# Optimization experiments

Hardware: AMD Instinct MI355X
Metric: run time of the kernel (lower is better)

Reference implementation:

```python
import jax, jax.numpy as jnp
import numpy as np

B, DIN, H, NACT = 8192, 1025, 1024, 1026
NHEAD = 513  # npatches + STOP
K = 32       # kR = kS


def _make_seq(key, batch, n, k):
    k_idx, k_len = jax.random.split(key)
    # distinct indices per row: top-k of a random permutation
    perm = jnp.argsort(jax.random.uniform(k_idx, (batch, n)), axis=1)[:, :k]
    seq_len = jax.random.randint(k_len, (batch,), 1, k + 1).astype(jnp.int32)
    mask = jnp.arange(k)[None, :] < seq_len[:, None]
    seq_idx = jnp.where(mask, perm, -1).astype(jnp.int32)
    return seq_idx, seq_len


def setup_inputs() -> dict:
    key = jax.random.key(0)
    ks = jax.random.split(key, 8)
    state = jax.random.normal(ks[0], (B, DIN), dtype=jnp.float32)
    W0 = jax.random.normal(ks[1], (DIN, H), dtype=jnp.float32) * (2.0 / DIN) ** 0.5
    b0 = jnp.zeros((H,), jnp.float32)
    W1 = jax.random.normal(ks[2], (H, H), dtype=jnp.float32) * (2.0 / H) ** 0.5
    b1 = jnp.zeros((H,), jnp.float32)
    W2 = jax.random.normal(ks[3], (H, NACT), dtype=jnp.float32) * 0.01
    b2 = jnp.zeros((NACT,), jnp.float32)
    seq_idx_R, seq_len_R = _make_seq(ks[4], B, NHEAD, K)
    seq_idx_S, seq_len_S = _make_seq(ks[5], B, NHEAD, K)
    return {"state": state, "W0": W0, "b0": b0, "W1": W1, "b1": b1,
            "W2": W2, "b2": b2,
            "seq_idx_R": seq_idx_R, "seq_len_R": seq_len_R,
            "seq_idx_S": seq_idx_S, "seq_len_S": seq_len_S}


def _mlp(state, W0, b0, W1, b1, W2, b2):
    h = jax.nn.relu(state @ W0 + b0)
    h = jax.nn.relu(h @ W1 + b1)
    return h @ W2 + b2  # (B, NACT) logits


def _logprob_entropy_wo_replacement(logits, seq_idx, seq_len):
    # Faithful vectorized version of logprob_entropy_wo_replacement_batched.
    bsz, n = logits.shape
    col = jnp.arange(n)[None, :]
    neg_inf = jnp.float32(-jnp.inf)

    def step(carry, xs):
        remaining, logp, ent = carry          # (B,N) bool, (B,), (B,)
        t, idx_t = xs                          # scalar, (B,)
        active = t < seq_len                   # (B,)
        masked_logits = jnp.where(remaining, logits, neg_inf)
        lp = jax.nn.log_softmax(masked_logits, axis=-1)
        p = jnp.exp(lp)
        mp = jnp.where(remaining, p, 0.0)
        mlp_ = jnp.where(remaining, lp, 0.0)
        ent_step = -jnp.sum(mp * mlp_, axis=-1)
        ent = ent + jnp.where(active, ent_step, 0.0)
        valid = active & (idx_t >= 0)
        idx_safe = jnp.where(valid, idx_t, 0)
        g = jnp.take_along_axis(lp, idx_safe[:, None], axis=1)[:, 0]
        logp = logp + jnp.where(valid, g, 0.0)
        hit = (col == idx_safe[:, None]) & valid[:, None]
        remaining = remaining & ~hit
        return (remaining, logp, ent), None

    init = (jnp.ones((bsz, n), bool), jnp.zeros((bsz,), jnp.float32),
            jnp.zeros((bsz,), jnp.float32))
    ts = jnp.arange(seq_idx.shape[1], dtype=jnp.int32)
    (_, logp, ent), _ = jax.lax.scan(step, init, (ts, seq_idx.T))
    return logp, ent


def reference(state, W0, b0, W1, b1, W2, b2,
              seq_idx_R, seq_len_R, seq_idx_S, seq_len_S):
    x = _mlp(state, W0, b0, W1, b1, W2, b2)
    logpR, entR = _logprob_entropy_wo_replacement(x[:, :NHEAD], seq_idx_R, seq_len_R)
    logpS, entS = _logprob_entropy_wo_replacement(x[:, NHEAD:NHEAD + NHEAD], seq_idx_S, seq_len_S)
    # rows: [total logprob, total entropy] as in get_log_prob's (logpR+logpS, entR+entS)
    return jnp.stack([logpR + logpS, entR + entS], axis=0)  # (2, B)
```

## Files before the change

### kernel.cpp

```cpp
#include <hip/hip_runtime.h>
#include <cstdint>
#include <cstddef>

#define BATCH 8192
#define DIN   1025
#define HID   1024
#define NACT  1026
#define NHEAD 513
#define KSEL  32
#define KP0   1088
#define LGN   1024

typedef unsigned short u16;
typedef short bf16x8 __attribute__((ext_vector_type(8)));
typedef float f32x4 __attribute__((ext_vector_type(4)));

__device__ __forceinline__ u16 f2bf(float f) {
  unsigned u = __float_as_uint(f);
  u += 0x7fff + ((u >> 16) & 1);
  return (u16)(u >> 16);
}
__device__ __forceinline__ float bf2f(u16 h) {
  return __uint_as_float((unsigned)h << 16);
}

__device__ __forceinline__ void async_cp16(const u16* g, u16* l) {
  __builtin_amdgcn_global_load_lds((const __attribute__((address_space(1))) void*)g,
                                   (__attribute__((address_space(3))) void*)l,
                                   16, 0, 0);
}

__global__ __launch_bounds__(512) void k_cvt(const float* __restrict__ state,
    const float* __restrict__ W0, const float* __restrict__ W1,
    const float* __restrict__ W2,
    u16* __restrict__ As, u16* __restrict__ W0t, u16* __restrict__ W1t,
    u16* __restrict__ W2t, u16* __restrict__ W2c) {
  const int tid = threadIdx.x;
  const int b = blockIdx.x;
  {
    int i = b * 512 + tid;
    const int QPR = KP0 / 4;
    int r = i / QPR, c4 = (i - r * QPR) * 4;
    const float* src = state + (size_t)r * DIN + c4;
    ushort4 o;
    if (c4 + 3 < DIN) {
      o.x = f2bf(src[0]); o.y = f2bf(src[1]); o.z = f2bf(src[2]); o.w = f2bf(src[3]);
    } else {
      o.x = (c4 + 0 < DIN) ? f2bf(src[0]) : 0;
      o.y = (c4 + 1 < DIN) ? f2bf(src[1]) : 0;
      o.z = (c4 + 2 < DIN) ? f2bf(src[2]) : 0;
      o.w = (c4 + 3 < DIN) ? f2bf(src[3]) : 0;
    }
    *(ushort4*)(As + (size_t)r * KP0 + c4) = o;
  }
  if (b >= 3137) return;
  if (b == 3136) {
    for (int e = tid; e < 2048; e += 512) {
      int j = e >> 10, k = e & 1023;
      W2c[e] = f2bf(W2[(size_t)k * NACT + 1024 + j]);
    }
    return;
  }
  const float* W; u16* Wt; int K, ldW, Kp, tt = b;
  if (tt < 1088)      { W = W0; Wt = W0t; K = DIN; ldW = HID;  Kp = KP0; }
  else if (tt < 2112) { tt -= 1088; W = W1; Wt = W1t; K = HID; ldW = HID;  Kp = HID; }
  else                { tt -= 2112; W = W2; Wt = W2t; K = HID; ldW = NACT; Kp = HID; }
  int n0 = (tt & 31) * 32, k0 = (tt >> 5) * 32;
  __shared__ float tile[32][33];
  const int tx = tid & 31, ty = tid >> 5;
#pragma unroll
  for (int i = 0; i < 32; i += 16) {
    int k = k0 + ty + i;
    tile[ty + i][tx] = (k < K) ? W[(size_t)k * ldW + n0 + tx] : 0.f;
  }
  __syncthreads();
#pragma unroll
  for (int i = 0; i < 32; i += 16)
    Wt[(size_t)(n0 + ty + i) * Kp + k0 + tx] = f2bf(tile[tx][ty + i]);
}

template<bool RELU, int K>
__global__ __launch_bounds__(256, 4)
void gemm_bt(const u16* __restrict__ A, const u16* __restrict__ Bt,
             const float* __restrict__ bias, u16* __restrict__ Cout, int ldc)
{
  __shared__ __align__(16) u16 lds[12288];

  const int d     = blockIdx.x;
  const int xcd   = d & 7;
  const int j     = d >> 3;
  const int mtile = (xcd << 3) | (j & 7);
  const int ntile = j >> 3;
  const size_t bm = (size_t)mtile * 128;
  const size_t bn = (size_t)ntile * 64;

  const int tid  = threadIdx.x;
  const int wave = tid >> 6;
  const int lane = tid & 63;
  const int waveM = wave >> 1, waveN = wave & 1;
  const int lr = lane & 15, lq = lane >> 4;

  const int row0 = tid >> 2;
  const int g_   = (tid & 3) ^ ((tid >> 3) & 3);
  const u16* gA0 = A  + (bm + row0) * (size_t)K + g_ * 8;
  const u16* gA1 = A  + (bm + row0 + 64) * (size_t)K + g_ * 8;
  const u16* gB0 = Bt + (bn + row0) * (size_t)K + g_ * 8;
  u16* lA0 = lds + wave * 512;
  u16* lA1 = lds + 2048 + wave * 512;
  u16* lB0 = lds + 4096 + wave * 512;

  f32x4 acc[4][2] = {};

  const int s = lq ^ ((lr >> 1) & 3);
  const u16* pa = lds + (waveM * 64 + lr) * 32 + s * 8;
  const u16* pb = lds + 4096 + (waveN * 32 + lr) * 32 + s * 8;

  auto issue = [&](int k0, int buf) {
    const int o = buf * 6144;
    async_cp16(gA0 + k0, lA0 + o);
    async_cp16(gA1 + k0, lA1 + o);
    async_cp16(gB0 + k0, lB0 + o);
  };

  const int NIT = K / 32;
  issue(0, 0);
#pragma unroll 2
  for (int it = 0; it < NIT; ++it) {
    const int buf = it & 1;
    if (it + 1 < NIT) {
      issue((it + 1) * 32, buf ^ 1);
      asm volatile("s_waitcnt vmcnt(3)\n\ts_barrier" ::: "memory");
    } else {
      asm volatile("s_waitcnt vmcnt(0)\n\ts_barrier" ::: "memory");
    }

    bf16x8 af[4], bfr[2];
    const u16* qa = pa + buf * 6144;
    const u16* qb = pb + buf * 6144;
#pragma unroll
    for (int t = 0; t < 4; ++t)
      af[t]  = *(const bf16x8*)(qa + t * 512);
#pragma unroll
    for (int t = 0; t < 2; ++t)
      bfr[t] = *(const bf16x8*)(qb + t * 512);
#pragma unroll
    for (int tm = 0; tm < 4; ++tm)
#pragma unroll
      for (int tn = 0; tn < 2; ++tn)
        acc[tm][tn] = __builtin_amdgcn_mfma_f32_16x16x32_bf16(af[tm], bfr[tn], acc[tm][tn], 0, 0, 0);

    asm volatile("s_waitcnt lgkmcnt(0)\n\ts_barrier" ::: "memory");
  }

#pragma unroll
  for (int tm = 0; tm < 4; ++tm) {
    size_t rw = bm + waveM * 64 + tm * 16 + lq * 4;
#pragma unroll
    for (int tn = 0; tn < 2; ++tn) {
      int col = (int)bn + waveN * 32 + tn * 16 + lr;
      float bv = bias[col];
#pragma unroll
      for (int r = 0; r < 4; ++r) {
        float v = acc[tm][tn][r] + bv;
        if (RELU) v = fmaxf(v, 0.f);
        Cout[(rw + r) * ldc + col] = f2bf(v);
      }
    }
  }
}

__global__ __launch_bounds__(512) void k_sample(const u16* __restrict__ lgts,
    const u16* __restrict__ h2, const u16* __restrict__ W2c,
    const float* __restrict__ b2,
    const int* __restrict__ idxR, const int* __restrict__ lenR,
    const int* __restrict__ idxS, const int* __restrict__ lenS,
    float* __restrict__ out) {
  __shared__ float shf[16];
  const int tid = threadIdx.x;
  const int w = tid >> 6, lane = tid & 63;
  const int grp = w & 1, pair = w >> 1;
  const int row = blockIdx.x * 4 + pair;
  const u16* base = lgts + (size_t)row * LGN + (grp ? NHEAD : 0);
  const int* sidx = (grp ? idxS : idxR) + (size_t)row * KSEL;
  const int slen  = (grp ? lenS : lenR)[row];

  float x1024 = 0.f, x1025 = 0.f;
  if (grp) {
    const bf16x8* hp  = (const bf16x8*)(h2 + (size_t)row * HID + lane * 16);
    const bf16x8* w0p = (const bf16x8*)(W2c + lane * 16);
    const bf16x8* w1p = (const bf16x8*)(W2c + 1024 + lane * 16);
    bf16x8 hv0 = hp[0],  hv1 = hp[1];
    bf16x8 a0  = w0p[0], a1  = w0p[1];
    bf16x8 c0  = w1p[0], c1  = w1p[1];
    float d0 = 0.f, d1 = 0.f;
#pragma unroll
    for (int j = 0; j < 8; ++j) {
      float h0 = bf2f((u16)hv0[j]);
      float h1 = bf2f((u16)hv1[j]);
      d0 += h0 * bf2f((u16)a0[j]) + h1 * bf2f((u16)a1[j]);
      d1 += h0 * bf2f((u16)c0[j]) + h1 * bf2f((u16)c1[j]);
    }
#pragma unroll
    for (int dd = 32; dd; dd >>= 1) { d0 += __shfl_xor(d0, dd, 64); d1 += __shfl_xor(d1, dd, 64); }
    x1024 = d0 + b2[1024];
    x1025 = d1 + b2[1025];
  }

  const u16* chunk = lgts + (size_t)row * LGN + (grp ? 512 : 0) + lane * 8;
  bf16x8 raw = *(const bf16x8*)chunk;
  float v[8];
#pragma unroll
  for (int j = 0; j < 8; ++j) v[j] = bf2f((u16)raw[j]);
  if (grp && lane == 0) v[0] = -3.4e38f;

  float xa = -3.4e38f; int has_xa = 0;
  if (!grp && lane == 0)  { xa = bf2f(base[512]); has_xa = 1; }
  if (grp  && lane == 63) { xa = x1024;           has_xa = 1; }
  if (grp  && lane == 0)  { xa = x1025;           has_xa = 1; }

  float m = -3.4e38f;
#pragma unroll
  for (int j = 0; j < 8; ++j) m = fmaxf(m, v[j]);
  if (has_xa) m = fmaxf(m, xa);
#pragma unroll
  for (int dd = 32; dd; dd >>= 1) m = fmaxf(m, __shfl_xor(m, dd, 64));

  float S = 0.f, T = 0.f;
#pragma unroll
  for (int j = 0; j < 8; ++j) {
    float e = __expf(v[j] - m);
    S += e; T += e * v[j];
  }
  if (has_xa) { float e = __expf(xa - m); S += e; T += e * xa; }
#pragma unroll
  for (int dd = 32; dd; dd >>= 1) { S += __shfl_xor(S, dd, 64); T += __shfl_xor(T, dd, 64); }

  float e = 0.f, ex = 0.f, xt = 0.f;
  int active = (lane < KSEL) && (lane < slen);
  int valid = 0;
  if (active) {
    int id = sidx[lane];
    if (id >= 0) {
      valid = 1;
      if (grp && id >= 511) xt = (id == 511) ? x1024 : x1025;
      else                  xt = bf2f(base[id]);
      e  = __expf(xt - m);
      ex = e * xt;
    }
  }
  float pe = e, pex = ex;
#pragma unroll
  for (int dd = 1; dd < 32; dd <<= 1) {
    float qa = __shfl_up(pe, dd, 64);
    float qb = __shfl_up(pex, dd, 64);
    if (lane >= dd) { pe += qa; pex += qb; }
  }
  float lp = 0.f, en = 0.f;
  if (active) {
    float St = S - (pe - e);
    float Tt = T - (pex - ex);
    float logZ = m + __logf(St);
    en = logZ - Tt / St;
    if (valid) lp = xt - logZ;
  }
#pragma unroll
  for (int dd = 32; dd; dd >>= 1) { lp += __shfl_xor(lp, dd, 64); en += __shfl_xor(en, dd, 64); }

  if (lane == 0) { shf[w * 2] = lp; shf[w * 2 + 1] = en; }
  __syncthreads();
  if (lane == 0 && grp == 0) {
    out[row]         = shf[pair * 4] + shf[pair * 4 + 2];
    out[BATCH + row] = shf[pair * 4 + 1] + shf[pair * 4 + 3];
  }
}

extern "C" void kernel_launch(void* const* d_in, const int* in_sizes, int n_in,
                              void* d_out, int out_size, void* d_ws, size_t ws_size,
                              hipStream_t stream) {
  (void)in_sizes; (void)n_in; (void)out_size; (void)ws_size;
  const float* state = (const float*)d_in[0];
  const float* W0 = (const float*)d_in[1];
  const float* b0 = (const float*)d_in[2];
  const float* W1 = (const float*)d_in[3];
  const float* b1 = (const float*)d_in[4];
  const float* W2 = (const float*)d_in[5];
  const float* b2 = (const float*)d_in[6];
  const int* idxR = (const int*)d_in[7];
  const int* lenR = (const int*)d_in[8];
  const int* idxS = (const int*)d_in[9];
  const int* lenS = (const int*)d_in[10];
  float* out = (float*)d_out;

  char* ws = (char*)d_ws;
  size_t off = 0;
  auto alloc = [&](size_t bytes) -> char* {
    char* p = ws + off;
    off = (off + bytes + 255) & ~(size_t)255;
    return p;
  };
  u16* As   = (u16*)alloc((size_t)BATCH * KP0 * 2);
  u16* W0t  = (u16*)alloc((size_t)HID * KP0 * 2);
  u16* W1t  = (u16*)alloc((size_t)HID * HID * 2);
  u16* W2t  = (u16*)alloc((size_t)HID * LGN * 2);
  u16* W2c  = (u16*)alloc((size_t)2 * 1024 * 2);
  u16* h1   = (u16*)alloc((size_t)BATCH * HID * 2);
  u16* h2   = (u16*)alloc((size_t)BATCH * HID * 2);
  u16* lgts = (u16*)alloc((size_t)BATCH * LGN * 2);

  k_cvt<<<4352, 512, 0, stream>>>(state, W0, W1, W2, As, W0t, W1t, W2t, W2c);

  gemm_bt<true,  KP0><<<1024, 256, 0, stream>>>(As, W0t, b0, h1,   HID);
  gemm_bt<true,  HID><<<1024, 256, 0, stream>>>(h1, W1t, b1, h2,   HID);
  gemm_bt<false, HID><<<1024, 256, 0, stream>>>(h2, W2t, b2, lgts, LGN);

  k_sample<<<2048, 512, 0, stream>>>(lgts, h2, W2c, b2, idxR, lenR, idxS, lenS, out);
}
```

Before: 209.2 us.

## Replace 128x64 GEMM tiles with 256x256 tiles and phased MFMA/prefetch schedule

The three MLP GEMMs move from 256-thread blocks computing 128x64 tiles to 512-thread blocks computing 256x256 tiles. The K step grows to 64, and a 128 KB double-buffered LDS holds both operands. The loop is split into four MFMA phases, each framed by barriers, raised wave priority and sched_barrier, with the next A and B async copies interleaved between phases. The aim is much higher operand reuse per LDS load and less global traffic. The cost is that only 128 blocks launch, fewer than the CU count, and the register and LDS footprint grows sharply.

```diff
diff --git a/kernel.cpp b/kernel.cpp
--- a/kernel.cpp
+++ b/kernel.cpp
@@ -80,90 +80,146 @@
 }
 
 template<bool RELU, int K>
-__global__ __launch_bounds__(256, 4)
-void gemm_bt(const u16* __restrict__ A, const u16* __restrict__ Bt,
+__global__ __launch_bounds__(512, 2)
+void gemm256(const u16* __restrict__ A, const u16* __restrict__ Bt,
              const float* __restrict__ bias, u16* __restrict__ Cout, int ldc)
 {
-  __shared__ __align__(16) u16 lds[12288];
-
-  const int d     = blockIdx.x;
-  const int xcd   = d & 7;
-  const int j     = d >> 3;
-  const int mtile = (xcd << 3) | (j & 7);
-  const int ntile = j >> 3;
-  const size_t bm = (size_t)mtile * 128;
-  const size_t bn = (size_t)ntile * 64;
+  __shared__ __align__(16) u16 lds[65536];
+
+  const int d = blockIdx.x;
+  const int wg    = (d & 7) * 16 + (d >> 3);
+  const int mtile = wg >> 2;
+  const int ntile = wg & 3;
+  const size_t bm = (size_t)mtile * 256;
+  const size_t bn = (size_t)ntile * 256;
 
   const int tid  = threadIdx.x;
   const int wave = tid >> 6;
   const int lane = tid & 63;
-  const int waveM = wave >> 1, waveN = wave & 1;
+  const int waveM = wave >> 2, waveN = wave & 3;
   const int lr = lane & 15, lq = lane >> 4;
-
-  const int row0 = tid >> 2;
-  const int g_   = (tid & 3) ^ ((tid >> 3) & 3);
-  const u16* gA0 = A  + (bm + row0) * (size_t)K + g_ * 8;
-  const u16* gA1 = A  + (bm + row0 + 64) * (size_t)K + g_ * 8;
-  const u16* gB0 = Bt + (bn + row0) * (size_t)K + g_ * 8;
-  u16* lA0 = lds + wave * 512;
-  u16* lA1 = lds + 2048 + wave * 512;
-  u16* lB0 = lds + 4096 + wave * 512;
-
-  f32x4 acc[4][2] = {};
-
-  const int s = lq ^ ((lr >> 1) & 3);
-  const u16* pa = lds + (waveM * 64 + lr) * 32 + s * 8;
-  const u16* pb = lds + 4096 + (waveN * 32 + lr) * 32 + s * 8;
-
-  auto issue = [&](int k0, int buf) {
-    const int o = buf * 6144;
-    async_cp16(gA0 + k0, lA0 + o);
-    async_cp16(gA1 + k0, lA1 + o);
-    async_cp16(gB0 + k0, lB0 + o);
-  };
-
-  const int NIT = K / 32;
-  issue(0, 0);
+  const int xr = lr & 7;
+
+  const int row0 = tid >> 3;
+  const int g_   = (tid & 7) ^ ((tid >> 3) & 7);
+  const u16* gA0 = A  + (bm + row0)       * (size_t)K + g_ * 8;
+  const u16* gA1 = A  + (bm + row0 + 64)  * (size_t)K + g_ * 8;
+  const u16* gA2 = A  + (bm + row0 + 128) * (size_t)K + g_ * 8;
+  const u16* gA3 = A  + (bm + row0 + 192) * (size_t)K + g_ * 8;
+  const u16* gB0 = Bt + (bn + row0)       * (size_t)K + g_ * 8;
+  const u16* gB1 = Bt + (bn + row0 + 64)  * (size_t)K + g_ * 8;
+  const u16* gB2 = Bt + (bn + row0 + 128) * (size_t)K + g_ * 8;
+  const u16* gB3 = Bt + (bn + row0 + 192) * (size_t)K + g_ * 8;
+  u16* lA = lds + wave * 512;
+  u16* lB = lds + 16384 + wave * 512;
+
+  const u16* paA = lds + (waveM * 128 + lr) * 64;
+  const u16* paB = lds + 16384 + (waveN * 64 + lr) * 64;
+  const int s0 = ( lq      ^ xr) * 8;
+  const int s1 = ((4 | lq) ^ xr) * 8;
+
+  f32x4 acc[8][4] = {};
+  bf16x8 af[4], ag[4], bfr[4], bgr[4];
+
+  {
+    async_cp16(gA0, lA);            async_cp16(gA1, lA + 4096);
+    async_cp16(gA2, lA + 8192);     async_cp16(gA3, lA + 12288);
+    async_cp16(gB0, lB);            async_cp16(gB1, lB + 4096);
+    async_cp16(gB2, lB + 8192);     async_cp16(gB3, lB + 12288);
+    asm volatile("s_waitcnt vmcnt(0)" ::: "memory");
+    __builtin_amdgcn_s_barrier();
+  }
+
+  const int NIT = K / 64;
 #pragma unroll 2
   for (int it = 0; it < NIT; ++it) {
-    const int buf = it & 1;
-    if (it + 1 < NIT) {
-      issue((it + 1) * 32, buf ^ 1);
-      asm volatile("s_waitcnt vmcnt(3)\n\ts_barrier" ::: "memory");
-    } else {
-      asm volatile("s_waitcnt vmcnt(0)\n\ts_barrier" ::: "memory");
-    }
-
-    bf16x8 af[4], bfr[2];
-    const u16* qa = pa + buf * 6144;
-    const u16* qb = pb + buf * 6144;
-#pragma unroll
-    for (int t = 0; t < 4; ++t)
-      af[t]  = *(const bf16x8*)(qa + t * 512);
-#pragma unroll
-    for (int t = 0; t < 2; ++t)
-      bfr[t] = *(const bf16x8*)(qb + t * 512);
-#pragma unroll
-    for (int tm = 0; tm < 4; ++tm)
-#pragma unroll
-      for (int tn = 0; tn < 2; ++tn)
-        acc[tm][tn] = __builtin_amdgcn_mfma_f32_16x16x32_bf16(af[tm], bfr[tn], acc[tm][tn], 0, 0, 0);
-
-    asm volatile("s_waitcnt lgkmcnt(0)\n\ts_barrier" ::: "memory");
-  }
-
-#pragma unroll
-  for (int tm = 0; tm < 4; ++tm) {
-    size_t rw = bm + waveM * 64 + tm * 16 + lq * 4;
-#pragma unroll
-    for (int tn = 0; tn < 2; ++tn) {
-      int col = (int)bn + waveN * 32 + tn * 16 + lr;
+    const int bo  = (it & 1) ? 32768 : 0;
+    const int bo2 = 32768 - bo;
+    const int kn  = (it + 1) * 64;
+    const bool pf = (it + 1 < NIT);
+
+#pragma unroll
+    for (int nf = 0; nf < 4; ++nf) bfr[nf] = *(const bf16x8*)(paB + bo + nf * 1024 + s0);
+#pragma unroll
+    for (int mf = 0; mf < 4; ++mf) af[mf]  = *(const bf16x8*)(paA + bo + mf * 1024 + s0);
+    if (pf) {
+      async_cp16(gA0 + kn, lA + bo2);         async_cp16(gA1 + kn, lA + bo2 + 4096);
+      async_cp16(gA2 + kn, lA + bo2 + 8192);  async_cp16(gA3 + kn, lA + bo2 + 12288);
+    }
+    __builtin_amdgcn_s_barrier();
+    asm volatile("s_waitcnt lgkmcnt(0)" ::: "memory");
+    __builtin_amdgcn_sched_barrier(0);
+    __builtin_amdgcn_s_setprio(1);
+#pragma unroll
+    for (int mf = 0; mf < 4; ++mf)
+#pragma unroll
+      for (int nf = 0; nf < 4; ++nf)
+        acc[mf][nf] = __builtin_amdgcn_mfma_f32_16x16x32_bf16(af[mf], bfr[nf], acc[mf][nf], 0, 0, 0);
+    __builtin_amdgcn_s_setprio(0);
+    __builtin_amdgcn_s_barrier();
+
+#pragma unroll
+    for (int mf = 0; mf < 4; ++mf) ag[mf] = *(const bf16x8*)(paA + bo + (mf + 4) * 1024 + s0);
+    if (pf) {
+      async_cp16(gB0 + kn, lB + bo2);         async_cp16(gB1 + kn, lB + bo2 + 4096);
+      async_cp16(gB2 + kn, lB + bo2 + 8192);  async_cp16(gB3 + kn, lB + bo2 + 12288);
+    }
+    __builtin_amdgcn_s_barrier();
+    asm volatile("s_waitcnt lgkmcnt(0)" ::: "memory");
+    __builtin_amdgcn_sched_barrier(0);
+    __builtin_amdgcn_s_setprio(1);
+#pragma unroll
+    for (int mf = 0; mf < 4; ++mf)
+#pragma unroll
+      for (int nf = 0; nf < 4; ++nf)
+        acc[mf + 4][nf] = __builtin_amdgcn_mfma_f32_16x16x32_bf16(ag[mf], bfr[nf], acc[mf + 4][nf], 0, 0, 0);
+    __builtin_amdgcn_s_setprio(0);
+    __builtin_amdgcn_s_barrier();
+
+#pragma unroll
+    for (int nf = 0; nf < 4; ++nf) bgr[nf] = *(const bf16x8*)(paB + bo + nf * 1024 + s1);
+#pragma unroll
+    for (int mf = 0; mf < 4; ++mf) af[mf]  = *(const bf16x8*)(paA + bo + mf * 1024 + s1);
+    __builtin_amdgcn_s_barrier();
+    asm volatile("s_waitcnt lgkmcnt(0)" ::: "memory");
+    __builtin_amdgcn_sched_barrier(0);
+    __builtin_amdgcn_s_setprio(1);
+#pragma unroll
+    for (int mf = 0; mf < 4; ++mf)
+#pragma unroll
+      for (int nf = 0; nf < 4; ++nf)
+        acc[mf][nf] = __builtin_amdgcn_mfma_f32_16x16x32_bf16(af[mf], bgr[nf], acc[mf][nf], 0, 0, 0);
+    __builtin_amdgcn_s_setprio(0);
+    __builtin_amdgcn_s_barrier();
+
+#pragma unroll
+    for (int mf = 0; mf < 4; ++mf) ag[mf] = *(const bf16x8*)(paA + bo + (mf + 4) * 1024 + s1);
+    __builtin_amdgcn_s_barrier();
+    asm volatile("s_waitcnt lgkmcnt(0)" ::: "memory");
+    __builtin_amdgcn_sched_barrier(0);
+    __builtin_amdgcn_s_setprio(1);
+#pragma unroll
+    for (int mf = 0; mf < 4; ++mf)
+#pragma unroll
+      for (int nf = 0; nf < 4; ++nf)
+        acc[mf + 4][nf] = __builtin_amdgcn_mfma_f32_16x16x32_bf16(ag[mf], bgr[nf], acc[mf + 4][nf], 0, 0, 0);
+    __builtin_amdgcn_s_setprio(0);
+    if (pf) asm volatile("s_waitcnt vmcnt(0)" ::: "memory");
+    __builtin_amdgcn_s_barrier();
+  }
+
+#pragma unroll
+  for (int mf = 0; mf < 8; ++mf) {
+    size_t rw = bm + waveM * 128 + mf * 16 + lq * 4;
+#pragma unroll
+    for (int nf = 0; nf < 4; ++nf) {
+      int col = (int)bn + waveN * 64 + nf * 16 + lr;
       float bv = bias[col];
 #pragma unroll
       for (int r = 0; r < 4; ++r) {
-        float v = acc[tm][tn][r] + bv;
+        float v = acc[mf][nf][r] + bv;
         if (RELU) v = fmaxf(v, 0.f);
-        Cout[(rw + r) * ldc + col] = f2bf(v);
+        Cout[(rw + r) * (size_t)ldc + col] = f2bf(v);
       }
     }
   }
@@ -309,9 +365,9 @@
 
   k_cvt<<<4352, 512, 0, stream>>>(state, W0, W1, W2, As, W0t, W1t, W2t, W2c);
 
-  gemm_bt<true,  KP0><<<1024, 256, 0, stream>>>(As, W0t, b0, h1,   HID);
-  gemm_bt<true,  HID><<<1024, 256, 0, stream>>>(h1, W1t, b1, h2,   HID);
-  gemm_bt<false, HID><<<1024, 256, 0, stream>>>(h2, W2t, b2, lgts, LGN);
+  gemm256<true,  KP0><<<128, 512, 0, stream>>>(As, W0t, b0, h1,   HID);
+  gemm256<true,  HID><<<128, 512, 0, stream>>>(h1, W1t, b1, h2,   HID);
+  gemm256<false, HID><<<128, 512, 0, stream>>>(h2, W2t, b2, lgts, LGN);
 
   k_sample<<<2048, 512, 0, stream>>>(lgts, h2, W2c, b2, idxR, lenR, idxS, lenS, out);
 }
```

New measurement: 216.5 us. +3.5%, slower.
